# Optimization experiments

Measured on AMD Instinct MI355X. Metric: run time of the kernel, lower is better.

## Reference

```python
import jax, jax.numpy as jnp
import numpy as np

H = 8          # num_heads
D = 64         # head_dim
HID = 512      # hidden_size
W = 128        # window_size
NEG = -1e9

def setup_inputs() -> dict:
    key = jax.random.key(0)
    ks = jax.random.split(key, 12)
    B, S = 2, 2048
    def lin(i):
        w = jax.random.normal(ks[i], (HID, HID), dtype=jnp.float32) * (1.0 / np.sqrt(HID))
        b = jax.random.normal(ks[i + 1], (HID,), dtype=jnp.float32) * 0.01
        return w, b
    Wq, bq = lin(0)
    Wk, bk = lin(2)
    Wv, bv = lin(4)
    Wo, bo = lin(6)
    return {
        "value": jax.random.normal(ks[8], (B, S, HID), dtype=jnp.float32),
        "key": jax.random.normal(ks[9], (B, S, HID), dtype=jnp.float32),
        "query": jax.random.normal(ks[10], (B, S, HID), dtype=jnp.float32),
        "Wq": Wq, "bq": bq, "Wk": Wk, "bk": bk,
        "Wv": Wv, "bv": bv, "Wo": Wo, "bo": bo,
    }

def reference(value, key, query, Wq, bq, Wk, bk, Wv, bv, Wo, bo):
    B, S, _ = query.shape
    def heads(x, Wt, b):
        # torch Linear: x @ W.T + b ; then [B,S,H,D] -> [B,H,S,D]
        return (x @ Wt.T + b).reshape(B, S, H, D).transpose(0, 2, 1, 3)
    Q = heads(query, Wq, bq)
    K = heads(key, Wk, bk)
    V = heads(value, Wv, bv)
    scores = jnp.einsum('bhqd,bhkd->bhqk', Q, K) / jnp.sqrt(jnp.float32(D))
    idx = jnp.arange(S)
    local = jnp.abs(idx[:, None] - idx[None, :]) <= W  # [S,S] band mask
    scores = jnp.where(local[None, None], scores, NEG)
    weights = jax.nn.softmax(scores, axis=-1)
    out = jnp.einsum('bhqk,bhkd->bhqd', weights, V)
    out = out.transpose(0, 2, 1, 3).reshape(B, S, HID)
    return out @ Wo.T + bo
```

## Files before the change

kernel.cpp:

```cpp
#include <hip/hip_runtime.h>
#include <stdint.h>

#define B_   2
#define S_   2048
#define H_   8
#define D_   64
#define HID_ 512
#define W_   128
#define M_   (B_ * S_)
#define E_   (M_ * HID_)
#define WE_  (HID_ * HID_)
#define PPAD_ 72
#define M0_  12.0f

typedef unsigned short u16;
typedef __attribute__((ext_vector_type(8))) __bf16 bf16x8;
typedef __attribute__((ext_vector_type(4))) float  floatx4;

__device__ __forceinline__ float b2f(u16 u) {
    union { unsigned int i; float f; } x;
    x.i = ((unsigned int)u) << 16;
    return x.f;
}
__device__ __forceinline__ u16 f2b(float f) {
    union { float f; unsigned int i; } x;
    x.f = f;
    unsigned int r = x.i + 0x7FFFu + ((x.i >> 16) & 1u);
    return (u16)(r >> 16);
}

__device__ __forceinline__ void gll16(const u16* g, u16* l) {
    __builtin_amdgcn_global_load_lds(
        (const __attribute__((address_space(1))) unsigned int*)g,
        (__attribute__((address_space(3))) unsigned int*)l, 16, 0, 0);
}

__global__ __launch_bounds__(256) void split_kernel(
    const float* __restrict__ q, const float* __restrict__ k, const float* __restrict__ v,
    const float* __restrict__ wq, const float* __restrict__ wk,
    const float* __restrict__ wv, const float* __restrict__ wo,
    u16* __restrict__ U) {
    const int y = blockIdx.y;
    const float* src;
    u16* dst;
    int n;
    if (y < 3) {
        src = (y == 0) ? q : (y == 1) ? k : v;
        dst = U + (size_t)y * E_;
        n = E_;
    } else {
        src = (y == 3) ? wq : (y == 4) ? wk : (y == 5) ? wv : wo;
        dst = U + 3 * (size_t)E_ + (size_t)(y - 3) * WE_;
        n = WE_;
    }
    const int idx = (blockIdx.x * 256 + threadIdx.x) * 4;
    if (idx >= n) return;
    const float4 x = *(const float4*)(src + idx);
    ushort4 hs;
    hs.x = f2b(x.x); hs.y = f2b(x.y); hs.z = f2b(x.z); hs.w = f2b(x.w);
    *(ushort4*)(dst + idx) = hs;
}

template <int MODE, int PASSES>
__device__ __forceinline__ void gemm_mfma_body(
    const u16* __restrict__ Xh, const u16* __restrict__ Xl,
    const u16* __restrict__ Wh, const float* __restrict__ bias,
    float* __restrict__ outF, u16* __restrict__ outH) {
    __shared__ u16 As[PASSES * 128 * 32];
    __shared__ u16 Bs[64 * 32];

    const int tid  = threadIdx.x;
    const int wave = tid >> 6;
    const int lane = tid & 63;
    const int r16  = lane & 15;
    const int quad = lane >> 4;
    const int lrow = lane >> 2;
    const int lk   = (lane & 3) * 8;
    const int m0 = blockIdx.x * 128;
    const int n0 = blockIdx.y * 64;
    const int m_base = m0 + wave * 64;

    floatx4 zero = {0.f, 0.f, 0.f, 0.f};
    floatx4 acc[4][4];
#pragma unroll
    for (int i = 0; i < 4; i++)
#pragma unroll
        for (int j = 0; j < 4; j++) acc[i][j] = zero;

    for (int k0 = 0; k0 < HID_; k0 += 32) {
        __syncthreads();
#pragma unroll
        for (int e = 0; e < 4; e++) {
            const int row = wave * 64 + e * 16 + lrow;
            const size_t go = (size_t)(m0 + row) * HID_ + k0 + lk;
            gll16(Xh + go, &As[(wave * 64 + e * 16) * 32]);
            if (PASSES == 2) gll16(Xl + go, &As[4096 + (wave * 64 + e * 16) * 32]);
        }
#pragma unroll
        for (int e = 0; e < 2; e++) {
            const int er = wave * 2 + e;
            const size_t go = (size_t)(n0 + er * 16 + lrow) * HID_ + k0 + lk;
            gll16(Wh + go, &Bs[(er * 16) * 32]);
        }
        __syncthreads();

        bf16x8 a0[4], a1[4], b[4];
#pragma unroll
        for (int t = 0; t < 4; t++) {
            const int ao = (wave * 64 + t * 16 + r16) * 32 + quad * 8;
            const int bo = (t * 16 + r16) * 32 + quad * 8;
            a0[t] = *(const bf16x8*)&As[ao];
            if (PASSES == 2) a1[t] = *(const bf16x8*)&As[4096 + ao];
            b[t]  = *(const bf16x8*)&Bs[bo];
        }
#pragma unroll
        for (int i = 0; i < 4; i++)
#pragma unroll
            for (int j = 0; j < 4; j++) {
                acc[i][j] = __builtin_amdgcn_mfma_f32_16x16x32_bf16(a0[i], b[j], acc[i][j], 0, 0, 0);
                if (PASSES == 2)
                    acc[i][j] = __builtin_amdgcn_mfma_f32_16x16x32_bf16(a1[i], b[j], acc[i][j], 0, 0, 0);
            }
    }

    const int bb = m_base >> 11;
    if (MODE == 0) {
#pragma unroll
        for (int j = 0; j < 4; j++) {
            const int col = n0 + j * 16 + r16;
            const float bv = bias[col];
#pragma unroll
            for (int i = 0; i < 4; i++) {
                const int row0 = m_base + i * 16 + quad * 4;
#pragma unroll
                for (int r = 0; r < 4; r++)
                    outF[(size_t)(row0 + r) * HID_ + col] = acc[i][j][r] + bv;
            }
        }
    } else if (MODE == 1) {
#pragma unroll
        for (int j = 0; j < 4; j++) {
            const int col = n0 + j * 16 + r16;
            const int h = col >> 6, d = col & (D_ - 1);
            const float bv = bias[col];
            const size_t base = (size_t)(bb * H_ + h) * S_;
#pragma unroll
            for (int i = 0; i < 4; i++)
#pragma unroll
                for (int r = 0; r < 4; r++) {
                    const int s = (m_base & (S_ - 1)) + i * 16 + quad * 4 + r;
                    outH[(base + s) * D_ + d] = f2b(acc[i][j][r] + bv);
                }
        }
    } else {
#pragma unroll
        for (int j = 0; j < 4; j++) {
            const int col = n0 + j * 16 + r16;
            const int h = col >> 6, d = col & (D_ - 1);
            const float bv = bias[col];
            const size_t base = ((size_t)(bb * H_ + h) * D_ + d) * S_;
            const int s0 = (m_base & (S_ - 1)) + quad * 4;
#pragma unroll
            for (int i = 0; i < 4; i++) {
                ushort4 hs;
                hs.x = f2b(acc[i][j][0] + bv);
                hs.y = f2b(acc[i][j][1] + bv);
                hs.z = f2b(acc[i][j][2] + bv);
                hs.w = f2b(acc[i][j][3] + bv);
                *(ushort4*)(outH + base + s0 + i * 16) = hs;
            }
        }
    }
}

__global__ __launch_bounds__(128) void qkv_mfma_kernel(
    const u16* __restrict__ U,
    const float* __restrict__ bq, const float* __restrict__ bk, const float* __restrict__ bv,
    u16* __restrict__ P) {
    const u16* Wb = U + 3 * (size_t)E_;
    if (blockIdx.z == 0)
        gemm_mfma_body<1, 1>(U, nullptr, Wb, bq, nullptr, P);
    else if (blockIdx.z == 1)
        gemm_mfma_body<1, 1>(U + E_, nullptr, Wb + WE_, bk, nullptr, P + E_);
    else
        gemm_mfma_body<2, 1>(U + 2 * (size_t)E_, nullptr, Wb + 2 * WE_, bv,
                             nullptr, P + 2 * (size_t)E_);
}

__global__ __launch_bounds__(128) void out_mfma_kernel(
    const u16* __restrict__ AOh, const u16* __restrict__ AOl,
    const u16* __restrict__ Woh, const float* __restrict__ bo,
    float* __restrict__ out) {
    gemm_mfma_body<0, 2>(AOh, AOl, Woh, bo, out, nullptr);
}

__global__ __launch_bounds__(256) void attn_kernel(
    const u16* __restrict__ Qh, const u16* __restrict__ Kh,
    const u16* __restrict__ Vth,
    u16* __restrict__ AOh, u16* __restrict__ AOl) {
    __shared__ u16   Ps[4][64][PPAD_];
    __shared__ float Ored[64][68];
    __shared__ float Lred[4][64];

    const int tid  = threadIdx.x;
    const int wave = tid >> 6;
    const int lane = tid & 63;
    const int r16 = lane & 15, quad = lane >> 4;
    const int qt = blockIdx.x, bh = blockIdx.y;
    const int q0 = qt * 64;
    const size_t sd = (size_t)bh * S_ * D_;
    const size_t ds = (size_t)bh * D_ * S_;

    floatx4 zero = {0.f, 0.f, 0.f, 0.f};
    floatx4 O[4][4];
    float lsum[4][4];
#pragma unroll
    for (int i = 0; i < 4; i++)
#pragma unroll
        for (int j = 0; j < 4; j++) O[i][j] = zero;
#pragma unroll
    for (int i = 0; i < 4; i++)
#pragma unroll
        for (int r = 0; r < 4; r++) lsum[i][r] = 0.f;

    int t_lo = qt - 2; if (t_lo < 0) t_lo = 0;
    int t_hi = qt + 2; if (t_hi > S_ / 64 - 1) t_hi = S_ / 64 - 1;

    for (int t = t_lo + wave; t <= t_hi; t += 4) {
        const int k0 = t * 64;
        floatx4 sa[4][4];
#pragma unroll
        for (int i = 0; i < 4; i++)
#pragma unroll
            for (int j = 0; j < 4; j++) sa[i][j] = zero;

#pragma unroll
        for (int ks = 0; ks < 2; ks++) {
            bf16x8 qf[4], kf[4];
#pragma unroll
            for (int i = 0; i < 4; i++)
                qf[i] = *(const bf16x8*)(Qh + sd + (size_t)(q0 + i * 16 + r16) * D_ + ks * 32 + quad * 8);
#pragma unroll
            for (int j = 0; j < 4; j++)
                kf[j] = *(const bf16x8*)(Kh + sd + (size_t)(k0 + j * 16 + r16) * D_ + ks * 32 + quad * 8);
#pragma unroll
            for (int i = 0; i < 4; i++)
#pragma unroll
                for (int j = 0; j < 4; j++)
                    sa[i][j] = __builtin_amdgcn_mfma_f32_16x16x32_bf16(qf[i], kf[j], sa[i][j], 0, 0, 0);
        }

#pragma unroll
        for (int i = 0; i < 4; i++)
#pragma unroll
            for (int j = 0; j < 4; j++) {
                const int kc = k0 + j * 16 + r16;
#pragma unroll
                for (int r = 0; r < 4; r++) {
                    const int q = q0 + i * 16 + quad * 4 + r;
                    const bool valid = (unsigned)(kc - q + W_) <= (unsigned)(2 * W_);
                    const float p = valid ? __expf(fmaf(sa[i][j][r], 0.125f, -M0_)) : 0.f;
                    lsum[i][r] += p;
                    Ps[wave][i * 16 + quad * 4 + r][j * 16 + r16] = f2b(p);
                }
            }

#pragma unroll
        for (int ks = 0; ks < 2; ks++) {
            bf16x8 pf[4], vf[4];
#pragma unroll
            for (int i = 0; i < 4; i++)
                pf[i] = *(const bf16x8*)&Ps[wave][i * 16 + r16][ks * 32 + quad * 8];
#pragma unroll
            for (int j = 0; j < 4; j++)
                vf[j] = *(const bf16x8*)(Vth + ds + (size_t)(j * 16 + r16) * S_ + k0 + ks * 32 + quad * 8);
#pragma unroll
            for (int i = 0; i < 4; i++)
#pragma unroll
                for (int j = 0; j < 4; j++)
                    O[i][j] = __builtin_amdgcn_mfma_f32_16x16x32_bf16(pf[i], vf[j], O[i][j], 0, 0, 0);
        }
    }

#pragma unroll
    for (int i = 0; i < 4; i++)
#pragma unroll
        for (int r = 0; r < 4; r++) {
            float l = lsum[i][r];
#pragma unroll
            for (int off = 1; off < 16; off <<= 1) l += __shfl_xor(l, off, 64);
            if (r16 == 0) Lred[wave][i * 16 + quad * 4 + r] = l;
        }

    const bool active = (t_lo + wave <= t_hi);
#pragma unroll
    for (int w = 0; w < 4; w++) {
        if (wave == w && active) {
#pragma unroll
            for (int i = 0; i < 4; i++)
#pragma unroll
                for (int j = 0; j < 4; j++) {
                    floatx4* cell = (floatx4*)&Ored[j * 16 + r16][i * 16 + quad * 4];
                    if (w == 0) *cell = O[i][j];
                    else        *cell = *cell + O[i][j];
                }
        }
        __syncthreads();
    }

    const int b = bh >> 3, h = bh & 7;
    const int q  = tid >> 2;
    const int d0 = (tid & 3) * 16;
    const float linv = 1.f / (Lred[0][q] + Lred[1][q] + Lred[2][q] + Lred[3][q]);
    const size_t base = (size_t)(b * S_ + q0 + q) * HID_ + h * D_ + d0;
#pragma unroll
    for (int k = 0; k < 16; k++) {
        const float v = Ored[d0 + k][q] * linv;
        const u16 hh = f2b(v);
        AOh[base + k] = hh;
        AOl[base + k] = f2b(v - b2f(hh));
    }
}

extern "C" void kernel_launch(void* const* d_in, const int* in_sizes, int n_in,
                              void* d_out, int out_size, void* d_ws, size_t ws_size,
                              hipStream_t stream) {
    const float* value = (const float*)d_in[0];
    const float* key_  = (const float*)d_in[1];
    const float* query = (const float*)d_in[2];
    const float* bq = (const float*)d_in[4];
    const float* bk = (const float*)d_in[6];
    const float* bv = (const float*)d_in[8];
    const float* bo = (const float*)d_in[10];

    u16* U = (u16*)d_ws;
    u16* P = U + 3 * (size_t)E_ + 4 * (size_t)WE_;
    u16* AOh = U;
    u16* AOl = U + E_;
    const u16* Wb = U + 3 * (size_t)E_;

    split_kernel<<<dim3(E_ / 1024, 7), 256, 0, stream>>>(
        query, key_, value,
        (const float*)d_in[3], (const float*)d_in[5],
        (const float*)d_in[7], (const float*)d_in[9], U);
    qkv_mfma_kernel<<<dim3(M_ / 128, HID_ / 64, 3), 128, 0, stream>>>(
        U, bq, bk, bv, P);
    attn_kernel<<<dim3(S_ / 64, B_ * H_), 256, 0, stream>>>(
        P, P + E_, P + 2 * (size_t)E_, AOh, AOl);
    out_mfma_kernel<<<dim3(M_ / 128, HID_ / 64), 128, 0, stream>>>(
        AOh, AOl, Wb + 3 * WE_, bo, (float*)d_out);
}
```

Baseline: 153.7 us.

## Double-buffer GEMM LDS tiles with BK=64 and four-wave blocks

Rewrites the shared MFMA GEMM body to double-buffer its LDS tiles. The next K=64 slab is prefetched while the current one is consumed, so there is one barrier per 64-wide K step instead of two per 32. Blocks grow to four waves, and the output projection uses smaller 64x32 tiles to launch more blocks. The aim is to hide global-load latency and raise occupancy, at the cost of more LDS per block and more work per wave.

```diff
diff --git a/kernel.cpp b/kernel.cpp
--- a/kernel.cpp
+++ b/kernel.cpp
@@ -61,76 +61,102 @@
     *(ushort4*)(dst + idx) = hs;
 }
 
-template <int MODE, int PASSES>
+template <int MODE, int PASSES, int BM, int BN>
 __device__ __forceinline__ void gemm_mfma_body(
     const u16* __restrict__ Xh, const u16* __restrict__ Xl,
     const u16* __restrict__ Wh, const float* __restrict__ bias,
     float* __restrict__ outF, u16* __restrict__ outH) {
-    __shared__ u16 As[PASSES * 128 * 32];
-    __shared__ u16 Bs[64 * 32];
+    constexpr int TM = BM / 64;
+    constexpr int TN = BN / 16;
+    constexpr int AGRP = BM / 16;
+    constexpr int BGRP = BN / 16;
+
+    __shared__ u16 As[2][PASSES][2][BM * 32];
+    __shared__ u16 Bs[2][2][BN * 32];
 
     const int tid  = threadIdx.x;
     const int wave = tid >> 6;
     const int lane = tid & 63;
     const int r16  = lane & 15;
     const int quad = lane >> 4;
-    const int lrow = lane >> 2;
-    const int lk   = (lane & 3) * 8;
-    const int m0 = blockIdx.x * 128;
-    const int n0 = blockIdx.y * 64;
-    const int m_base = m0 + wave * 64;
+    const int srow = lane >> 2;
+    const int sk   = (lane & 3) * 8;
+    const int m0 = blockIdx.x * BM;
+    const int n0 = blockIdx.y * BN;
 
     floatx4 zero = {0.f, 0.f, 0.f, 0.f};
-    floatx4 acc[4][4];
-#pragma unroll
-    for (int i = 0; i < 4; i++)
-#pragma unroll
-        for (int j = 0; j < 4; j++) acc[i][j] = zero;
-
-    for (int k0 = 0; k0 < HID_; k0 += 32) {
+    floatx4 acc[TM][TN];
+#pragma unroll
+    for (int i = 0; i < TM; i++)
+#pragma unroll
+        for (int j = 0; j < TN; j++) acc[i][j] = zero;
+
+    auto stage = [&](int buf, int k0) {
+        int slot = 0;
+#pragma unroll
+        for (int p = 0; p < PASSES; p++)
+#pragma unroll
+            for (int ks = 0; ks < 2; ks++)
+#pragma unroll
+                for (int g = 0; g < AGRP; g++, slot++)
+                    if ((slot & 3) == wave) {
+                        const u16* src = (p ? Xl : Xh) +
+                            (size_t)(m0 + g * 16 + srow) * HID_ + k0 + ks * 32 + sk;
+                        gll16(src, &As[buf][p][ks][g * 16 * 32]);
+                    }
+#pragma unroll
+        for (int ks = 0; ks < 2; ks++)
+#pragma unroll
+            for (int g = 0; g < BGRP; g++, slot++)
+                if ((slot & 3) == wave) {
+                    const u16* src = Wh +
+                        (size_t)(n0 + g * 16 + srow) * HID_ + k0 + ks * 32 + sk;
+                    gll16(src, &Bs[buf][ks][g * 16 * 32]);
+                }
+    };
+
+    stage(0, 0);
+    constexpr int NIT = HID_ / 64;
+    for (int it = 0; it < NIT; it++) {
         __syncthreads();
-#pragma unroll
-        for (int e = 0; e < 4; e++) {
-            const int row = wave * 64 + e * 16 + lrow;
-            const size_t go = (size_t)(m0 + row) * HID_ + k0 + lk;
-            gll16(Xh + go, &As[(wave * 64 + e * 16) * 32]);
-            if (PASSES == 2) gll16(Xl + go, &As[4096 + (wave * 64 + e * 16) * 32]);
-        }
-#pragma unroll
-        for (int e = 0; e < 2; e++) {
-            const int er = wave * 2 + e;
-            const size_t go = (size_t)(n0 + er * 16 + lrow) * HID_ + k0 + lk;
-            gll16(Wh + go, &Bs[(er * 16) * 32]);
-        }
-        __syncthreads();
-
-        bf16x8 a0[4], a1[4], b[4];
-#pragma unroll
-        for (int t = 0; t < 4; t++) {
-            const int ao = (wave * 64 + t * 16 + r16) * 32 + quad * 8;
-            const int bo = (t * 16 + r16) * 32 + quad * 8;
-            a0[t] = *(const bf16x8*)&As[ao];
-            if (PASSES == 2) a1[t] = *(const bf16x8*)&As[4096 + ao];
-            b[t]  = *(const bf16x8*)&Bs[bo];
-        }
-#pragma unroll
-        for (int i = 0; i < 4; i++)
-#pragma unroll
-            for (int j = 0; j < 4; j++) {
-                acc[i][j] = __builtin_amdgcn_mfma_f32_16x16x32_bf16(a0[i], b[j], acc[i][j], 0, 0, 0);
-                if (PASSES == 2)
-                    acc[i][j] = __builtin_amdgcn_mfma_f32_16x16x32_bf16(a1[i], b[j], acc[i][j], 0, 0, 0);
-            }
-    }
-
+        if (it + 1 < NIT) stage((it + 1) & 1, (it + 1) * 64);
+        const int buf = it & 1;
+
+        bf16x8 bfr[2][TN];
+#pragma unroll
+        for (int ks = 0; ks < 2; ks++)
+#pragma unroll
+            for (int j = 0; j < TN; j++)
+                bfr[ks][j] = *(const bf16x8*)&Bs[buf][ks][(j * 16 + r16) * 32 + quad * 8];
+#pragma unroll
+        for (int p = 0; p < PASSES; p++) {
+            bf16x8 afr[2][TM];
+#pragma unroll
+            for (int ks = 0; ks < 2; ks++)
+#pragma unroll
+                for (int i = 0; i < TM; i++)
+                    afr[ks][i] = *(const bf16x8*)
+                        &As[buf][p][ks][(wave * TM * 16 + i * 16 + r16) * 32 + quad * 8];
+#pragma unroll
+            for (int ks = 0; ks < 2; ks++)
+#pragma unroll
+                for (int i = 0; i < TM; i++)
+#pragma unroll
+                    for (int j = 0; j < TN; j++)
+                        acc[i][j] = __builtin_amdgcn_mfma_f32_16x16x32_bf16(
+                            afr[ks][i], bfr[ks][j], acc[i][j], 0, 0, 0);
+        }
+    }
+
+    const int m_base = m0 + wave * TM * 16;
     const int bb = m_base >> 11;
     if (MODE == 0) {
 #pragma unroll
-        for (int j = 0; j < 4; j++) {
+        for (int j = 0; j < TN; j++) {
             const int col = n0 + j * 16 + r16;
             const float bv = bias[col];
 #pragma unroll
-            for (int i = 0; i < 4; i++) {
+            for (int i = 0; i < TM; i++) {
                 const int row0 = m_base + i * 16 + quad * 4;
 #pragma unroll
                 for (int r = 0; r < 4; r++)
@@ -139,13 +165,13 @@
         }
     } else if (MODE == 1) {
 #pragma unroll
-        for (int j = 0; j < 4; j++) {
+        for (int j = 0; j < TN; j++) {
             const int col = n0 + j * 16 + r16;
             const int h = col >> 6, d = col & (D_ - 1);
             const float bv = bias[col];
             const size_t base = (size_t)(bb * H_ + h) * S_;
 #pragma unroll
-            for (int i = 0; i < 4; i++)
+            for (int i = 0; i < TM; i++)
 #pragma unroll
                 for (int r = 0; r < 4; r++) {
                     const int s = (m_base & (S_ - 1)) + i * 16 + quad * 4 + r;
@@ -154,14 +180,14 @@
         }
     } else {
 #pragma unroll
-        for (int j = 0; j < 4; j++) {
+        for (int j = 0; j < TN; j++) {
             const int col = n0 + j * 16 + r16;
             const int h = col >> 6, d = col & (D_ - 1);
             const float bv = bias[col];
             const size_t base = ((size_t)(bb * H_ + h) * D_ + d) * S_;
             const int s0 = (m_base & (S_ - 1)) + quad * 4;
 #pragma unroll
-            for (int i = 0; i < 4; i++) {
+            for (int i = 0; i < TM; i++) {
                 ushort4 hs;
                 hs.x = f2b(acc[i][j][0] + bv);
                 hs.y = f2b(acc[i][j][1] + bv);
@@ -173,25 +199,25 @@
     }
 }
 
-__global__ __launch_bounds__(128) void qkv_mfma_kernel(
+__global__ __launch_bounds__(256) void qkv_mfma_kernel(
     const u16* __restrict__ U,
     const float* __restrict__ bq, const float* __restrict__ bk, const float* __restrict__ bv,
     u16* __restrict__ P) {
     const u16* Wb = U + 3 * (size_t)E_;
     if (blockIdx.z == 0)
-        gemm_mfma_body<1, 1>(U, nullptr, Wb, bq, nullptr, P);
+        gemm_mfma_body<1, 1, 128, 64>(U, nullptr, Wb, bq, nullptr, P);
     else if (blockIdx.z == 1)
-        gemm_mfma_body<1, 1>(U + E_, nullptr, Wb + WE_, bk, nullptr, P + E_);
+        gemm_mfma_body<1, 1, 128, 64>(U + E_, nullptr, Wb + WE_, bk, nullptr, P + E_);
     else
-        gemm_mfma_body<2, 1>(U + 2 * (size_t)E_, nullptr, Wb + 2 * WE_, bv,
-                             nullptr, P + 2 * (size_t)E_);
-}
-
-__global__ __launch_bounds__(128) void out_mfma_kernel(
+        gemm_mfma_body<2, 1, 128, 64>(U + 2 * (size_t)E_, nullptr, Wb + 2 * WE_, bv,
+                                      nullptr, P + 2 * (size_t)E_);
+}
+
+__global__ __launch_bounds__(256) void out_mfma_kernel(
     const u16* __restrict__ AOh, const u16* __restrict__ AOl,
     const u16* __restrict__ Woh, const float* __restrict__ bo,
     float* __restrict__ out) {
-    gemm_mfma_body<0, 2>(AOh, AOl, Woh, bo, out, nullptr);
+    gemm_mfma_body<0, 2, 64, 32>(AOh, AOl, Woh, bo, out, nullptr);
 }
 
 __global__ __launch_bounds__(256) void attn_kernel(
@@ -343,10 +369,10 @@
         query, key_, value,
         (const float*)d_in[3], (const float*)d_in[5],
         (const float*)d_in[7], (const float*)d_in[9], U);
-    qkv_mfma_kernel<<<dim3(M_ / 128, HID_ / 64, 3), 128, 0, stream>>>(
+    qkv_mfma_kernel<<<dim3(M_ / 128, HID_ / 64, 3), 256, 0, stream>>>(
         U, bq, bk, bv, P);
     attn_kernel<<<dim3(S_ / 64, B_ * H_), 256, 0, stream>>>(
         P, P + E_, P + 2 * (size_t)E_, AOh, AOl);
-    out_mfma_kernel<<<dim3(M_ / 128, HID_ / 64), 128, 0, stream>>>(
+    out_mfma_kernel<<<dim3(M_ / 64, HID_ / 32), 256, 0, stream>>>(
         AOh, AOl, Wb + 3 * WE_, bo, (float*)d_out);
 }
```

Result: no change. 155.2 us (+1.0%).

## Fuse fp32-to-bf16 conversion into GEMM loads and drop hi/lo split

Applied to the files above, without the earlier changes.

Removes the standalone conversion kernel; the QKV and output projection GEMMs now load fp32 inputs/weights directly and convert to bf16 while staging into shared memory. The attention output is stored as a single bf16 value instead of a hi/lo pair, halving the output GEMM's MFMA passes. This cuts a launch and a full pass of global traffic, at the cost of synchronous (non-async) fp32 loads in the GEMMs and reduced precision in the output projection.

```diff
diff --git a/kernel.cpp b/kernel.cpp
--- a/kernel.cpp
+++ b/kernel.cpp
@@ -9,7 +9,6 @@
 #define W_   128
 #define M_   (B_ * S_)
 #define E_   (M_ * HID_)
-#define WE_  (HID_ * HID_)
 #define PPAD_ 72
 #define M0_  12.0f
 
@@ -35,38 +34,18 @@
         (__attribute__((address_space(3))) unsigned int*)l, 16, 0, 0);
 }
 
-__global__ __launch_bounds__(256) void split_kernel(
-    const float* __restrict__ q, const float* __restrict__ k, const float* __restrict__ v,
-    const float* __restrict__ wq, const float* __restrict__ wk,
-    const float* __restrict__ wv, const float* __restrict__ wo,
-    u16* __restrict__ U) {
-    const int y = blockIdx.y;
-    const float* src;
-    u16* dst;
-    int n;
-    if (y < 3) {
-        src = (y == 0) ? q : (y == 1) ? k : v;
-        dst = U + (size_t)y * E_;
-        n = E_;
-    } else {
-        src = (y == 3) ? wq : (y == 4) ? wk : (y == 5) ? wv : wo;
-        dst = U + 3 * (size_t)E_ + (size_t)(y - 3) * WE_;
-        n = WE_;
-    }
-    const int idx = (blockIdx.x * 256 + threadIdx.x) * 4;
-    if (idx >= n) return;
-    const float4 x = *(const float4*)(src + idx);
-    ushort4 hs;
-    hs.x = f2b(x.x); hs.y = f2b(x.y); hs.z = f2b(x.z); hs.w = f2b(x.w);
-    *(ushort4*)(dst + idx) = hs;
-}
-
-template <int MODE, int PASSES>
-__device__ __forceinline__ void gemm_mfma_body(
-    const u16* __restrict__ Xh, const u16* __restrict__ Xl,
-    const u16* __restrict__ Wh, const float* __restrict__ bias,
-    float* __restrict__ outF, u16* __restrict__ outH) {
-    __shared__ u16 As[PASSES * 128 * 32];
+__device__ __forceinline__ void cvt8_store(float4 a, float4 b, u16* dst) {
+    bf16x8 v;
+    v[0] = (__bf16)a.x; v[1] = (__bf16)a.y; v[2] = (__bf16)a.z; v[3] = (__bf16)a.w;
+    v[4] = (__bf16)b.x; v[5] = (__bf16)b.y; v[6] = (__bf16)b.z; v[7] = (__bf16)b.w;
+    *(bf16x8*)dst = v;
+}
+
+template <int MODE>
+__device__ __forceinline__ void gemm_fp32in_body(
+    const float* __restrict__ Xf, const float* __restrict__ Wf,
+    const float* __restrict__ bias, u16* __restrict__ outH) {
+    __shared__ u16 As[128 * 32];
     __shared__ u16 Bs[64 * 32];
 
     const int tid  = threadIdx.x;
@@ -74,12 +53,15 @@
     const int lane = tid & 63;
     const int r16  = lane & 15;
     const int quad = lane >> 4;
-    const int lrow = lane >> 2;
-    const int lk   = (lane & 3) * 8;
     const int m0 = blockIdx.x * 128;
     const int n0 = blockIdx.y * 64;
     const int m_base = m0 + wave * 64;
 
+    const int ar = tid >> 2;
+    const int ak = (tid & 3) * 8;
+    const int br = tid >> 1;
+    const int bk2 = (tid & 1) * 16;
+
     floatx4 zero = {0.f, 0.f, 0.f, 0.f};
     floatx4 acc[4][4];
 #pragma unroll
@@ -91,53 +73,32 @@
         __syncthreads();
 #pragma unroll
         for (int e = 0; e < 4; e++) {
-            const int row = wave * 64 + e * 16 + lrow;
-            const size_t go = (size_t)(m0 + row) * HID_ + k0 + lk;
-            gll16(Xh + go, &As[(wave * 64 + e * 16) * 32]);
-            if (PASSES == 2) gll16(Xl + go, &As[4096 + (wave * 64 + e * 16) * 32]);
-        }
-#pragma unroll
-        for (int e = 0; e < 2; e++) {
-            const int er = wave * 2 + e;
-            const size_t go = (size_t)(n0 + er * 16 + lrow) * HID_ + k0 + lk;
-            gll16(Wh + go, &Bs[(er * 16) * 32]);
-        }
-        __syncthreads();
-
-        bf16x8 a0[4], a1[4], b[4];
+            const int row = e * 32 + ar;
+            const float4* src = (const float4*)(Xf + (size_t)(m0 + row) * HID_ + k0 + ak);
+            cvt8_store(src[0], src[1], &As[row * 32 + ak]);
+        }
+        {
+            const float4* src = (const float4*)(Wf + (size_t)(n0 + br) * HID_ + k0 + bk2);
+            cvt8_store(src[0], src[1], &Bs[br * 32 + bk2]);
+            cvt8_store(src[2], src[3], &Bs[br * 32 + bk2 + 8]);
+        }
+        __syncthreads();
+
+        bf16x8 a0[4], b[4];
 #pragma unroll
         for (int t = 0; t < 4; t++) {
-            const int ao = (wave * 64 + t * 16 + r16) * 32 + quad * 8;
-            const int bo = (t * 16 + r16) * 32 + quad * 8;
-            a0[t] = *(const bf16x8*)&As[ao];
-            if (PASSES == 2) a1[t] = *(const bf16x8*)&As[4096 + ao];
-            b[t]  = *(const bf16x8*)&Bs[bo];
+            a0[t] = *(const bf16x8*)&As[(wave * 64 + t * 16 + r16) * 32 + quad * 8];
+            b[t]  = *(const bf16x8*)&Bs[(t * 16 + r16) * 32 + quad * 8];
         }
 #pragma unroll
         for (int i = 0; i < 4; i++)
 #pragma unroll
-            for (int j = 0; j < 4; j++) {
+            for (int j = 0; j < 4; j++)
                 acc[i][j] = __builtin_amdgcn_mfma_f32_16x16x32_bf16(a0[i], b[j], acc[i][j], 0, 0, 0);
-                if (PASSES == 2)
-                    acc[i][j] = __builtin_amdgcn_mfma_f32_16x16x32_bf16(a1[i], b[j], acc[i][j], 0, 0, 0);
-            }
     }
 
     const int bb = m_base >> 11;
-    if (MODE == 0) {
-#pragma unroll
-        for (int j = 0; j < 4; j++) {
-            const int col = n0 + j * 16 + r16;
-            const float bv = bias[col];
-#pragma unroll
-            for (int i = 0; i < 4; i++) {
-                const int row0 = m_base + i * 16 + quad * 4;
-#pragma unroll
-                for (int r = 0; r < 4; r++)
-                    outF[(size_t)(row0 + r) * HID_ + col] = acc[i][j][r] + bv;
-            }
-        }
-    } else if (MODE == 1) {
+    if (MODE == 1) {
 #pragma unroll
         for (int j = 0; j < 4; j++) {
             const int col = n0 + j * 16 + r16;
@@ -173,31 +134,87 @@
     }
 }
 
-__global__ __launch_bounds__(128) void qkv_mfma_kernel(
-    const u16* __restrict__ U,
+__global__ __launch_bounds__(128) void qkv_fused_kernel(
+    const float* __restrict__ xq, const float* __restrict__ xk, const float* __restrict__ xv,
+    const float* __restrict__ wq, const float* __restrict__ wk, const float* __restrict__ wv,
     const float* __restrict__ bq, const float* __restrict__ bk, const float* __restrict__ bv,
     u16* __restrict__ P) {
-    const u16* Wb = U + 3 * (size_t)E_;
-    if (blockIdx.z == 0)
-        gemm_mfma_body<1, 1>(U, nullptr, Wb, bq, nullptr, P);
-    else if (blockIdx.z == 1)
-        gemm_mfma_body<1, 1>(U + E_, nullptr, Wb + WE_, bk, nullptr, P + E_);
-    else
-        gemm_mfma_body<2, 1>(U + 2 * (size_t)E_, nullptr, Wb + 2 * WE_, bv,
-                             nullptr, P + 2 * (size_t)E_);
-}
-
-__global__ __launch_bounds__(128) void out_mfma_kernel(
-    const u16* __restrict__ AOh, const u16* __restrict__ AOl,
-    const u16* __restrict__ Woh, const float* __restrict__ bo,
-    float* __restrict__ out) {
-    gemm_mfma_body<0, 2>(AOh, AOl, Woh, bo, out, nullptr);
+    if (blockIdx.z == 0)      gemm_fp32in_body<1>(xq, wq, bq, P);
+    else if (blockIdx.z == 1) gemm_fp32in_body<1>(xk, wk, bk, P + E_);
+    else                      gemm_fp32in_body<2>(xv, wv, bv, P + 2 * (size_t)E_);
+}
+
+__global__ __launch_bounds__(128) void out_fused_kernel(
+    const u16* __restrict__ AOh, const float* __restrict__ Wf,
+    const float* __restrict__ bias, float* __restrict__ outF) {
+    __shared__ u16 As[128 * 32];
+    __shared__ u16 Bs[64 * 32];
+
+    const int tid  = threadIdx.x;
+    const int wave = tid >> 6;
+    const int lane = tid & 63;
+    const int r16  = lane & 15;
+    const int quad = lane >> 4;
+    const int lrow = lane >> 2;
+    const int lk   = (lane & 3) * 8;
+    const int br   = tid >> 1;
+    const int bk2  = (tid & 1) * 16;
+    const int m0 = blockIdx.x * 128;
+    const int n0 = blockIdx.y * 64;
+    const int m_base = m0 + wave * 64;
+
+    floatx4 zero = {0.f, 0.f, 0.f, 0.f};
+    floatx4 acc[4][4];
+#pragma unroll
+    for (int i = 0; i < 4; i++)
+#pragma unroll
+        for (int j = 0; j < 4; j++) acc[i][j] = zero;
+
+    for (int k0 = 0; k0 < HID_; k0 += 32) {
+        __syncthreads();
+#pragma unroll
+        for (int e = 0; e < 4; e++) {
+            const int row = wave * 64 + e * 16 + lrow;
+            gll16(AOh + (size_t)(m0 + row) * HID_ + k0 + lk,
+                  &As[(wave * 64 + e * 16) * 32]);
+        }
+        {
+            const float4* src = (const float4*)(Wf + (size_t)(n0 + br) * HID_ + k0 + bk2);
+            cvt8_store(src[0], src[1], &Bs[br * 32 + bk2]);
+            cvt8_store(src[2], src[3], &Bs[br * 32 + bk2 + 8]);
+        }
+        __syncthreads();
+
+        bf16x8 a0[4], b[4];
+#pragma unroll
+        for (int t = 0; t < 4; t++) {
+            a0[t] = *(const bf16x8*)&As[(wave * 64 + t * 16 + r16) * 32 + quad * 8];
+            b[t]  = *(const bf16x8*)&Bs[(t * 16 + r16) * 32 + quad * 8];
+        }
+#pragma unroll
+        for (int i = 0; i < 4; i++)
+#pragma unroll
+            for (int j = 0; j < 4; j++)
+                acc[i][j] = __builtin_amdgcn_mfma_f32_16x16x32_bf16(a0[i], b[j], acc[i][j], 0, 0, 0);
+    }
+
+#pragma unroll
+    for (int j = 0; j < 4; j++) {
+        const int col = n0 + j * 16 + r16;
+        const float bv = bias[col];
+#pragma unroll
+        for (int i = 0; i < 4; i++) {
+            const int row0 = m_base + i * 16 + quad * 4;
+#pragma unroll
+            for (int r = 0; r < 4; r++)
+                outF[(size_t)(row0 + r) * HID_ + col] = acc[i][j][r] + bv;
+        }
+    }
 }
 
 __global__ __launch_bounds__(256) void attn_kernel(
     const u16* __restrict__ Qh, const u16* __restrict__ Kh,
-    const u16* __restrict__ Vth,
-    u16* __restrict__ AOh, u16* __restrict__ AOl) {
+    const u16* __restrict__ Vth, u16* __restrict__ AOh) {
     __shared__ u16   Ps[4][64][PPAD_];
     __shared__ float Ored[64][68];
     __shared__ float Lred[4][64];
@@ -314,12 +331,8 @@
     const float linv = 1.f / (Lred[0][q] + Lred[1][q] + Lred[2][q] + Lred[3][q]);
     const size_t base = (size_t)(b * S_ + q0 + q) * HID_ + h * D_ + d0;
 #pragma unroll
-    for (int k = 0; k < 16; k++) {
-        const float v = Ored[d0 + k][q] * linv;
-        const u16 hh = f2b(v);
-        AOh[base + k] = hh;
-        AOl[base + k] = f2b(v - b2f(hh));
-    }
+    for (int k = 0; k < 16; k++)
+        AOh[base + k] = f2b(Ored[d0 + k][q] * linv);
 }
 
 extern "C" void kernel_launch(void* const* d_in, const int* in_sizes, int n_in,
@@ -328,25 +341,22 @@
     const float* value = (const float*)d_in[0];
     const float* key_  = (const float*)d_in[1];
     const float* query = (const float*)d_in[2];
+    const float* Wq = (const float*)d_in[3];
     const float* bq = (const float*)d_in[4];
+    const float* Wk = (const float*)d_in[5];
     const float* bk = (const float*)d_in[6];
+    const float* Wv = (const float*)d_in[7];
     const float* bv = (const float*)d_in[8];
+    const float* Wo = (const float*)d_in[9];
     const float* bo = (const float*)d_in[10];
 
-    u16* U = (u16*)d_ws;
-    u16* P = U + 3 * (size_t)E_ + 4 * (size_t)WE_;
-    u16* AOh = U;
-    u16* AOl = U + E_;
-    const u16* Wb = U + 3 * (size_t)E_;
-
-    split_kernel<<<dim3(E_ / 1024, 7), 256, 0, stream>>>(
-        query, key_, value,
-        (const float*)d_in[3], (const float*)d_in[5],
-        (const float*)d_in[7], (const float*)d_in[9], U);
-    qkv_mfma_kernel<<<dim3(M_ / 128, HID_ / 64, 3), 128, 0, stream>>>(
-        U, bq, bk, bv, P);
+    u16* P   = (u16*)d_ws;
+    u16* AOh = P + 3 * (size_t)E_;
+
+    qkv_fused_kernel<<<dim3(M_ / 128, HID_ / 64, 3), 128, 0, stream>>>(
+        query, key_, value, Wq, Wk, Wv, bq, bk, bv, P);
     attn_kernel<<<dim3(S_ / 64, B_ * H_), 256, 0, stream>>>(
-        P, P + E_, P + 2 * (size_t)E_, AOh, AOl);
-    out_mfma_kernel<<<dim3(M_ / 128, HID_ / 64), 128, 0, stream>>>(
-        AOh, AOl, Wb + 3 * WE_, bo, (float*)d_out);
-}
+        P, P + E_, P + 2 * (size_t)E_, AOh);
+    out_fused_kernel<<<dim3(M_ / 128, HID_ / 64), 128, 0, stream>>>(
+        AOh, Wo, bo, (float*)d_out);
+}
```

Result: faster. 149.7 us (-2.6%).
